# Kernel optimization log

Hardware: AMD Instinct MI355X
Metric: run time of the kernel (lower is better)

## Reference

```python
import jax, jax.numpy as jnp
import numpy as np

N = 50000      # nodes
E = 400000     # edges (before self-loops)
IN = 128       # in_channels
OUT = 64       # out_channels (per-head; concat=False averages heads)
HEADS = 8      # heads of first GAT layer; second layer has 1 head
NEG_SLOPE = 0.2


def _glorot(key, shape, fan_in, fan_out):
    s = jnp.sqrt(2.0 / (fan_in + fan_out)).astype(jnp.float32)
    return jax.random.normal(key, shape, jnp.float32) * s


def setup_inputs() -> dict:
    key = jax.random.key(0)
    ks = jax.random.split(key, 10)
    x = jax.random.normal(ks[0], (N, IN), jnp.float32)
    edge_index = jax.random.randint(ks[1], (2, E), 0, N)
    # layer 1: heads=HEADS, per-head dim OUT
    W1 = _glorot(ks[2], (IN, HEADS * OUT), IN, HEADS * OUT)
    att_src1 = _glorot(ks[3], (HEADS, OUT), OUT, 1)
    att_dst1 = _glorot(ks[4], (HEADS, OUT), OUT, 1)
    b1 = jnp.zeros((OUT,), jnp.float32)
    # layer 2: heads=1
    W2 = _glorot(ks[5], (OUT, 1 * OUT), OUT, OUT)
    att_src2 = _glorot(ks[6], (1, OUT), OUT, 1)
    att_dst2 = _glorot(ks[7], (1, OUT), OUT, 1)
    b2 = jnp.zeros((OUT,), jnp.float32)
    return dict(x=x, edge_index=edge_index, W1=W1, att_src1=att_src1,
                att_dst1=att_dst1, b1=b1, W2=W2, att_src2=att_src2,
                att_dst2=att_dst2, b2=b2)


def gat_conv(x, edge_index, W, att_src, att_dst, bias, heads, ch):
    """PyG GATConv with concat=False (mean over heads), add_self_loops=True."""
    n = x.shape[0]
    loop = jnp.arange(n, dtype=edge_index.dtype)
    src = jnp.concatenate([edge_index[0], loop])  # [E+N]
    dst = jnp.concatenate([edge_index[1], loop])
    h = (x @ W).reshape(n, heads, ch)                     # [N, H, C]
    a_s = jnp.sum(h * att_src, axis=-1)                   # [N, H]
    a_d = jnp.sum(h * att_dst, axis=-1)                   # [N, H]
    e = jax.nn.leaky_relu(a_s[src] + a_d[dst], NEG_SLOPE)  # [E+N, H]
    # numerically stable segment softmax over incoming edges of each dst node
    emax = jax.lax.stop_gradient(
        jax.ops.segment_max(e, dst, num_segments=n))       # [N, H]
    ee = jnp.exp(e - emax[dst])
    denom = jax.ops.segment_sum(ee, dst, num_segments=n)  # [N, H]
    alpha = ee / denom[dst]                                # [E+N, H]
    out = jax.ops.segment_sum(alpha[:, :, None] * h[src], dst,
                              num_segments=n)              # [N, H, C]
    return out.mean(axis=1) + bias                         # [N, C]


def reference(x, edge_index, W1, att_src1, att_dst1, b1,
              W2, att_src2, att_dst2, b2):
    h = gat_conv(x, edge_index, W1, att_src1, att_dst1, b1, HEADS, OUT)
    h = jax.nn.elu(h)
    return gat_conv(h, edge_index, W2, att_src2, att_dst2, b2, 1, OUT)
```

## Files before the change

kernel.cpp:

```cpp
#include <hip/hip_runtime.h>
#include <cstdint>
#include <cstddef>

#define NEG_SLOPE 0.2f

typedef short bf16x8 __attribute__((ext_vector_type(8)));
typedef float f32x4 __attribute__((ext_vector_type(4)));
typedef float f32x2 __attribute__((ext_vector_type(2)));

__device__ __forceinline__ unsigned short f2bf(float f) {
  unsigned u = __float_as_uint(f);
  u = u + 0x7FFFu + ((u >> 16) & 1u);
  return (unsigned short)(u >> 16);
}
__device__ __forceinline__ float bf2f(unsigned short b) {
  return __uint_as_float((unsigned)b << 16);
}
__device__ __forceinline__ f32x2 unpk(unsigned xv) {
  f32x2 r;
  r.x = __uint_as_float(xv << 16);
  r.y = __uint_as_float(xv & 0xFFFF0000u);
  return r;
}
__device__ __forceinline__ float rlf(float v, int l) {
  return __uint_as_float(
      (unsigned)__builtin_amdgcn_readlane((int)__float_as_uint(v), l));
}
__device__ __forceinline__ void dma16(const unsigned short* g, unsigned short* l) {
  __builtin_amdgcn_global_load_lds(
      (const __attribute__((address_space(1))) unsigned*)g,
      (__attribute__((address_space(3))) unsigned*)l, 16, 0, 0);
}

__global__ __launch_bounds__(256) void prep_all(
    const int* __restrict__ ei, int* __restrict__ counts,
    const float* __restrict__ x, unsigned short* __restrict__ xb,
    const float* __restrict__ W1, const float* __restrict__ att_s1,
    const float* __restrict__ att_d1, unsigned short* __restrict__ AsAdT,
    unsigned short* __restrict__ WbT,
    const float* __restrict__ W2, unsigned short* __restrict__ W2t,
    const float* __restrict__ att_s2, const float* __restrict__ att_d2,
    float* __restrict__ AsAd2,
    int E, int ET, int N, int B0, int B1) {
  int b = blockIdx.x, tid = threadIdx.x;
  if (b < B0) {
    int i = b * 256 + tid;
    if (i < ET) {
      int dst = (i < E) ? ei[E + i] : (i - E);
      atomicAdd(&counts[dst], 1);
    }
    return;
  }
  b -= B0;
  if (b < B1) {
    int i = b * 256 + tid;
    if (i < N * 32) {
      float4 v = ((const float4*)x)[i];
      ushort4 o;
      o.x = f2bf(v.x); o.y = f2bf(v.y); o.z = f2bf(v.z); o.w = f2bf(v.w);
      ((ushort4*)xb)[i] = o;
    }
    return;
  }
  b -= B1;
  if (b < 8) {
    int i = b * 256 + tid;
    int o = i >> 7, k = i & 127, h = o & 7;
    const float* att = (o < 8) ? att_s1 : att_d1;
    float s = 0.f;
    for (int c = 0; c < 64; c++) s += W1[(size_t)k * 512 + h * 64 + c] * att[h * 64 + c];
    AsAdT[i] = f2bf(s);
    return;
  }
  b -= 8;
  if (b < 256) {
    int i = b * 256 + tid;
    int o = i >> 10, k = i & 1023, h = k >> 7, c = k & 127;
    WbT[i] = f2bf(W1[(size_t)c * 512 + h * 64 + o]);
    return;
  }
  b -= 256;
  if (b < 16) {
    int i = b * 256 + tid;
    if (i < 64 * 64) {
      int k = i >> 6, nn = i & 63;
      W2t[(size_t)nn * 64 + k] = f2bf(W2[i]);
    }
    return;
  }
  {
    int i = tid;
    if (i < 128) {
      int o = i >> 6, k = i & 63;
      const float* att = (o == 0) ? att_s2 : att_d2;
      float s = 0.f;
      for (int c = 0; c < 64; c++) s += W2[(size_t)k * 64 + c] * att[c];
      AsAd2[i] = s;
    }
  }
}

__global__ __launch_bounds__(1024) void scan_dots(
    const int* __restrict__ counts, int* __restrict__ offsets,
    const unsigned short* __restrict__ xb, const unsigned short* __restrict__ AsAdT,
    float* __restrict__ asd, int n) {
  if (blockIdx.x == 0) {
    __shared__ int sums[1024];
    int t = threadIdx.x;
    int chunk = (n + 1023) >> 10;
    int start = t * chunk;
    int end = min(start + chunk, n);
    int s = 0;
    for (int i = start; i < end; i++) s += counts[i];
    sums[t] = s;
    __syncthreads();
    for (int off = 1; off < 1024; off <<= 1) {
      int v = (t >= off) ? sums[t - off] : 0;
      __syncthreads();
      sums[t] += v;
      __syncthreads();
    }
    int run = sums[t] - s;
    for (int i = start; i < end; i++) { offsets[i] = run; run += counts[i]; }
    if (t == 1023) offsets[n] = sums[1023];
    return;
  }
  int tid = threadIdx.x;
  int wave = tid >> 6, lane = tid & 63;
  int q = lane >> 4, t = lane & 15;
  int row0 = (blockIdx.x - 1) * 256 + wave * 16;
  int arow = row0 + t; if (arow > n - 1) arow = n - 1;
  const bf16x8* aptr = (const bf16x8*)(xb + (size_t)arow * 128);
  const bf16x8* bptr = (const bf16x8*)(AsAdT + t * 128);
  f32x4 acc = (f32x4){0.f, 0.f, 0.f, 0.f};
  #pragma unroll
  for (int s = 0; s < 4; s++)
    acc = __builtin_amdgcn_mfma_f32_16x16x32_bf16(aptr[s * 4 + q], bptr[s * 4 + q],
                                                  acc, 0, 0, 0);
  #pragma unroll
  for (int r = 0; r < 4; r++) {
    int row = row0 + q * 4 + r;
    if (row < n) asd[row * 16 + t] = acc[r];
  }
}

__global__ __launch_bounds__(256) void fill_csr(
    const int* __restrict__ ei, const int* __restrict__ offsets,
    int* __restrict__ cursor, int* __restrict__ srcs, int E, int ET) {
  int i = blockIdx.x * 256 + threadIdx.x;
  if (i >= ET) return;
  int src, dst;
  if (i < E) { src = ei[i]; dst = ei[E + i]; } else { src = dst = i - E; }
  int pos = atomicAdd(&cursor[dst], 1);
  srcs[offsets[dst] + pos] = src;
}

__global__ __launch_bounds__(1024, 8) void agg1_gemm(
    const int* __restrict__ offsets, const int* __restrict__ srcs,
    const float* __restrict__ asd, const unsigned short* __restrict__ xb,
    const unsigned short* __restrict__ WbT, const float* __restrict__ b1,
    const float* __restrict__ AsAd2, unsigned short* __restrict__ zb,
    float* __restrict__ as2, float* __restrict__ ad2, int N) {
  __shared__ unsigned short sh[16 * 2048];
  int tid = threadIdx.x;
  int wv = tid >> 6, lane = tid & 63;
  int nb = blockIdx.x;
  {
    int node = nb * 16 + wv;
    unsigned short* stg = &sh[wv * 2048];
    f32x2 acc[8];
    #pragma unroll
    for (int h = 0; h < 8; h++) acc[h] = (f32x2){0.f, 0.f};
    float wsl = 0.f;
    int beg = offsets[node], end = offsets[node + 1];
    int jl = end - 1;
    float adv = asd[(size_t)node * 16 + 8 + (lane & 7)];
    int s0 = srcs[min(beg + (lane >> 4), jl)];
    int s1 = srcs[min(beg + 4 + (lane >> 4), jl)];
    int s2 = 0, s3 = 0;
    float asva, asvb = 0.f;
    {
      int swa = srcs[min(beg + (lane >> 3), jl)];
      asva = asd[(size_t)swa * 16 + (lane & 7)];
    }
    if (end - beg > 8) {
      s2 = srcs[min(beg + 8 + (lane >> 4), jl)];
      s3 = srcs[min(beg + 12 + (lane >> 4), jl)];
      int swb = srcs[min(beg + 8 + (lane >> 3), jl)];
      asvb = asd[(size_t)swb * 16 + (lane & 7)];
    }
    for (int cb = beg; cb < end; cb += 16) {
      int rem = end - cb;
      bool bigh = rem > 8;
      dma16(xb + (size_t)s0 * 128 + (lane & 15) * 8, stg);
      dma16(xb + (size_t)s1 * 128 + (lane & 15) * 8, stg + 512);
      if (bigh) {
        dma16(xb + (size_t)s2 * 128 + (lane & 15) * 8, stg + 1024);
        dma16(xb + (size_t)s3 * 128 + (lane & 15) * 8, stg + 1536);
      }
      float wa, wb = 0.f;
      {
        float v = asva + adv;
        v = (v > 0.f) ? v : NEG_SLOPE * v;
        wa = (cb + (lane >> 3) < end) ? __expf(v) : 0.f;
      }
      if (bigh) {
        float v = asvb + adv;
        v = (v > 0.f) ? v : NEG_SLOPE * v;
        wb = (cb + 8 + (lane >> 3) < end) ? __expf(v) : 0.f;
      }
      wsl += wa + wb;
      int cn = cb + 16;
      if (cn < end) {
        s0 = srcs[min(cn + (lane >> 4), jl)];
        s1 = srcs[min(cn + 4 + (lane >> 4), jl)];
        int swa = srcs[min(cn + (lane >> 3), jl)];
        asva = asd[(size_t)swa * 16 + (lane & 7)];
        if (end - cn > 8) {
          s2 = srcs[min(cn + 8 + (lane >> 4), jl)];
          s3 = srcs[min(cn + 12 + (lane >> 4), jl)];
          int swb = srcs[min(cn + 8 + (lane >> 3), jl)];
          asvb = asd[(size_t)swb * 16 + (lane & 7)];
        }
      }
      __builtin_amdgcn_s_waitcnt(0x0f70);
      #pragma unroll
      for (int k = 0; k < 8; k++) {
        unsigned xv = *(const unsigned*)&stg[k * 128 + 2 * lane];
        f32x2 x2 = unpk(xv);
        acc[0] += x2 * rlf(wa, k * 8 + 0);
        acc[1] += x2 * rlf(wa, k * 8 + 1);
        acc[2] += x2 * rlf(wa, k * 8 + 2);
        acc[3] += x2 * rlf(wa, k * 8 + 3);
        acc[4] += x2 * rlf(wa, k * 8 + 4);
        acc[5] += x2 * rlf(wa, k * 8 + 5);
        acc[6] += x2 * rlf(wa, k * 8 + 6);
        acc[7] += x2 * rlf(wa, k * 8 + 7);
      }
      if (bigh) {
        #pragma unroll
        for (int k = 0; k < 8; k++) {
          unsigned xv = *(const unsigned*)&stg[1024 + k * 128 + 2 * lane];
          f32x2 x2 = unpk(xv);
          acc[0] += x2 * rlf(wb, k * 8 + 0);
          acc[1] += x2 * rlf(wb, k * 8 + 1);
          acc[2] += x2 * rlf(wb, k * 8 + 2);
          acc[3] += x2 * rlf(wb, k * 8 + 3);
          acc[4] += x2 * rlf(wb, k * 8 + 4);
          acc[5] += x2 * rlf(wb, k * 8 + 5);
          acc[6] += x2 * rlf(wb, k * 8 + 6);
          acc[7] += x2 * rlf(wb, k * 8 + 7);
        }
      }
    }
    wsl += __shfl_xor(wsl, 8, 64);
    wsl += __shfl_xor(wsl, 16, 64);
    wsl += __shfl_xor(wsl, 32, 64);
    __syncthreads();
    #pragma unroll
    for (int h = 0; h < 8; h++) {
      float tot = rlf(wsl, h);
      float iv = 0.125f / tot;
      unsigned o = (unsigned)f2bf(acc[h].x * iv) | ((unsigned)f2bf(acc[h].y * iv) << 16);
      *(unsigned*)&sh[wv * 1032 + h * 128 + 2 * lane] = o;
    }
  }
  __syncthreads();
  if (wv < 4) {
    int q = lane >> 4, t = lane & 15;
    f32x4 acc4 = (f32x4){0.f, 0.f, 0.f, 0.f};
    const unsigned short* bbase = WbT + (size_t)(wv * 16 + t) * 1024;
    #pragma unroll 8
    for (int s = 0; s < 32; s++) {
      bf16x8 af = *(const bf16x8*)&sh[t * 1032 + s * 32 + q * 8];
      bf16x8 bf = *(const bf16x8*)&bbase[s * 32 + q * 8];
      acc4 = __builtin_amdgcn_mfma_f32_16x16x32_bf16(af, bf, acc4, 0, 0, 0);
    }
    int col = wv * 16 + t;
    float bias = b1[col];
    float vs = AsAd2[col], vd = AsAd2[64 + col];
    #pragma unroll
    for (int r = 0; r < 4; r++) {
      int row = q * 4 + r;
      int node = nb * 16 + row;
      float v = acc4[r] + bias;
      v = (v > 0.f) ? v : (__expf(v) - 1.f);
      zb[(size_t)node * 64 + col] = f2bf(v);
      float s = v * vs, d = v * vd;
      #pragma unroll
      for (int off = 1; off < 16; off <<= 1) {
        s += __shfl_xor(s, off, 64);
        d += __shfl_xor(d, off, 64);
      }
      if (t == 0) {
        atomicAdd(&as2[node], s);
        atomicAdd(&ad2[node], d);
      }
    }
  }
}

__global__ __launch_bounds__(1024, 8) void agg2_gemm(
    const int* __restrict__ offsets, const int* __restrict__ srcs,
    const float* __restrict__ as2, const float* __restrict__ ad2,
    const unsigned short* __restrict__ zb, const unsigned short* __restrict__ W2t,
    const float* __restrict__ b2, float* __restrict__ out, int N) {
  __shared__ unsigned short sh[16 * 72];
  __shared__ int ssrc[16][64];
  int tid = threadIdx.x;
  int wv = tid >> 6, lane = tid & 63;
  int nb = blockIdx.x;
  {
    int row = wv;
    int node = nb * 16 + row;
    int half = lane >> 5;
    int l2 = lane & 31;
    float adv = ad2[node];
    int beg = offsets[node], end = offsets[node + 1];
    f32x2 acc = (f32x2){0.f, 0.f};
    float ws = 0.f;
    for (int cb = beg; cb < end; cb += 64) {
      int cnt = min(64, end - cb);
      if (lane < cnt) ssrc[row][lane] = srcs[cb + lane];
      #pragma unroll 2
      for (int k = half; k < cnt; k += 2) {
        int s = ssrc[row][k];
        float asv = as2[s];
        unsigned zv = *(const unsigned*)&zb[(size_t)s * 64 + 2 * l2];
        float v = asv + adv;
        v = (v > 0.f) ? v : NEG_SLOPE * v;
        float w = __expf(v);
        ws += w;
        acc += unpk(zv) * w;
      }
    }
    acc.x += __shfl_xor(acc.x, 32, 64);
    acc.y += __shfl_xor(acc.y, 32, 64);
    ws += __shfl_xor(ws, 32, 64);
    if (half == 0) {
      float inv = 1.f / ws;
      unsigned o = (unsigned)f2bf(acc.x * inv) | ((unsigned)f2bf(acc.y * inv) << 16);
      *(unsigned*)&sh[row * 72 + 2 * l2] = o;
    }
  }
  __syncthreads();
  if (wv < 4) {
    int q = lane >> 4, t = lane & 15;
    f32x4 acc4 = (f32x4){0.f, 0.f, 0.f, 0.f};
    const unsigned short* bbase = W2t + (size_t)(wv * 16 + t) * 64;
    #pragma unroll
    for (int s = 0; s < 2; s++) {
      bf16x8 af = *(const bf16x8*)&sh[t * 72 + s * 32 + q * 8];
      bf16x8 bf = *(const bf16x8*)&bbase[s * 32 + q * 8];
      acc4 = __builtin_amdgcn_mfma_f32_16x16x32_bf16(af, bf, acc4, 0, 0, 0);
    }
    int col = wv * 16 + t;
    float bias = b2[col];
    #pragma unroll
    for (int r = 0; r < 4; r++) {
      int node = nb * 16 + q * 4 + r;
      if (node < N) out[(size_t)node * 64 + col] = acc4[r] + bias;
    }
  }
}

extern "C" void kernel_launch(void* const* d_in, const int* in_sizes, int n_in,
                              void* d_out, int out_size, void* d_ws, size_t ws_size,
                              hipStream_t stream) {
  const int IN = 128;
  const int N = in_sizes[0] / IN;
  const int E = in_sizes[1] / 2;
  const int ET = E + N;

  const float* x        = (const float*)d_in[0];
  const int*   ei       = (const int*)d_in[1];
  const float* W1       = (const float*)d_in[2];
  const float* att_src1 = (const float*)d_in[3];
  const float* att_dst1 = (const float*)d_in[4];
  const float* b1       = (const float*)d_in[5];
  const float* W2       = (const float*)d_in[6];
  const float* att_src2 = (const float*)d_in[7];
  const float* att_dst2 = (const float*)d_in[8];
  const float* b2       = (const float*)d_in[9];
  float* out = (float*)d_out;

  char* base = (char*)d_ws;
  size_t off = 0;
  auto alloc = [&](size_t bytes) -> char* {
    char* p = base + off;
    off = (off + bytes + 255) & ~(size_t)255;
    return p;
  };
  unsigned short* xb    = (unsigned short*)alloc((size_t)N * 128 * 2);
  unsigned short* AsAdT = (unsigned short*)alloc((size_t)16 * 128 * 2);
  unsigned short* WbT   = (unsigned short*)alloc((size_t)64 * 1024 * 2);
  unsigned short* W2t   = (unsigned short*)alloc((size_t)64 * 64 * 2);
  unsigned short* zb    = (unsigned short*)alloc((size_t)N * 64 * 2);
  float* AsAd2 = (float*)alloc((size_t)128 * 4);
  float* asd1  = (float*)alloc((size_t)N * 16 * 4);
  int* offsets = (int*)alloc((size_t)(N + 1) * 4);
  int* srcs    = (int*)alloc((size_t)ET * 4);
  char* zero_begin = base + off;
  int* counts  = (int*)alloc((size_t)N * 4);
  int* cursor  = (int*)alloc((size_t)N * 4);
  float* a_s2  = (float*)alloc((size_t)N * 4);
  float* a_d2  = (float*)alloc((size_t)N * 4);
  char* zero_end = base + off;

  hipMemsetAsync(zero_begin, 0, (size_t)(zero_end - zero_begin), stream);

  const int TB = 256;
  auto cdiv = [](int a, int b) { return (a + b - 1) / b; };

  int B0 = cdiv(ET, TB);
  int B1 = cdiv(N * 32, TB);
  prep_all<<<B0 + B1 + 8 + 256 + 16 + 1, TB, 0, stream>>>(
      ei, counts, x, xb, W1, att_src1, att_dst1, AsAdT, WbT, W2, W2t,
      att_src2, att_dst2, AsAd2, E, ET, N, B0, B1);

  scan_dots<<<1 + cdiv(N, 256), 1024, 0, stream>>>(counts, offsets, xb, AsAdT,
                                                   asd1, N);

  fill_csr<<<cdiv(ET, TB), TB, 0, stream>>>(ei, offsets, cursor, srcs, E, ET);

  agg1_gemm<<<cdiv(N, 16), 1024, 0, stream>>>(offsets, srcs, asd1, xb, WbT, b1,
                                              AsAd2, zb, a_s2, a_d2, N);

  agg2_gemm<<<cdiv(N, 16), 1024, 0, stream>>>(offsets, srcs, a_s2, a_d2, zb,
                                              W2t, b2, out, N);
}
```

Measured before the change: 325.0 us.

## Stage layer-2 neighbor feature gathers through LDS via async DMA in 16-edge chunks

Rewrites the layer-2 aggregation loop so that each wave loads 16 source rows per chunk directly into LDS using asynchronous global-to-LDS copies. Each edge weight is computed once per lane and broadcast with lane reads, replacing the per-edge serial loads of srcs, as2 and zb. The goal is to raise memory-level parallelism and remove the dependent index load before each gather. In exchange it uses a large LDS staging buffer per block, which may cut occupancy, and it relies on correct waitcnt handling for the DMA.

```diff
diff --git a/kernel.cpp b/kernel.cpp
--- a/kernel.cpp
+++ b/kernel.cpp
@@ -305,42 +305,51 @@
     const float* __restrict__ as2, const float* __restrict__ ad2,
     const unsigned short* __restrict__ zb, const unsigned short* __restrict__ W2t,
     const float* __restrict__ b2, float* __restrict__ out, int N) {
+  __shared__ unsigned short stg[16 * 1024];
   __shared__ unsigned short sh[16 * 72];
-  __shared__ int ssrc[16][64];
   int tid = threadIdx.x;
   int wv = tid >> 6, lane = tid & 63;
   int nb = blockIdx.x;
   {
-    int row = wv;
-    int node = nb * 16 + row;
-    int half = lane >> 5;
-    int l2 = lane & 31;
+    int node = nb * 16 + wv;
+    unsigned short* st = &stg[wv * 1024];
     float adv = ad2[node];
     int beg = offsets[node], end = offsets[node + 1];
+    int jl = end - 1;
     f32x2 acc = (f32x2){0.f, 0.f};
-    float ws = 0.f;
-    for (int cb = beg; cb < end; cb += 64) {
-      int cnt = min(64, end - cb);
-      if (lane < cnt) ssrc[row][lane] = srcs[cb + lane];
-      #pragma unroll 2
-      for (int k = half; k < cnt; k += 2) {
-        int s = ssrc[row][k];
-        float asv = as2[s];
-        unsigned zv = *(const unsigned*)&zb[(size_t)s * 64 + 2 * l2];
-        float v = asv + adv;
-        v = (v > 0.f) ? v : NEG_SLOPE * v;
-        float w = __expf(v);
-        ws += w;
+    float wsl = 0.f;
+    for (int cb = beg; cb < end; cb += 16) {
+      int s0 = srcs[min(cb + (lane >> 3), jl)];
+      int s1 = srcs[min(cb + 8 + (lane >> 3), jl)];
+      int we = srcs[min(cb + (lane & 15), jl)];
+      float asv = as2[we];
+      dma16(zb + (size_t)s0 * 64 + (lane & 7) * 8, st);
+      dma16(zb + (size_t)s1 * 64 + (lane & 7) * 8, st + 512);
+      float v = asv + adv;
+      v = (v > 0.f) ? v : NEG_SLOPE * v;
+      float wl = (cb + (lane & 15) < end) ? __expf(v) : 0.f;
+      if (lane < 16) wsl += wl;
+      __builtin_amdgcn_s_waitcnt(0x0f70);
+      #pragma unroll
+      for (int k = 0; k < 8; k++) {
+        float w0 = rlf(wl, 2 * k);
+        float w1 = rlf(wl, 2 * k + 1);
+        float w = (lane >= 32) ? w1 : w0;
+        unsigned zv = *(const unsigned*)&st[(2 * k + (lane >> 5)) * 64 + 2 * (lane & 31)];
         acc += unpk(zv) * w;
       }
     }
+    wsl += __shfl_xor(wsl, 1, 64);
+    wsl += __shfl_xor(wsl, 2, 64);
+    wsl += __shfl_xor(wsl, 4, 64);
+    wsl += __shfl_xor(wsl, 8, 64);
+    float tot = rlf(wsl, 0);
     acc.x += __shfl_xor(acc.x, 32, 64);
     acc.y += __shfl_xor(acc.y, 32, 64);
-    ws += __shfl_xor(ws, 32, 64);
-    if (half == 0) {
-      float inv = 1.f / ws;
+    if (lane < 32) {
+      float inv = 1.f / tot;
       unsigned o = (unsigned)f2bf(acc.x * inv) | ((unsigned)f2bf(acc.y * inv) << 16);
-      *(unsigned*)&sh[row * 72 + 2 * l2] = o;
+      *(unsigned*)&sh[wv * 72 + 2 * lane] = o;
     }
   }
   __syncthreads();
```

Measured after the change: 326.3 us. Within noise of the previous version (+0.4%).
